# Kernel tuning notes

Measured on AMD Instinct MI355X. Metric: run time of the kernel, lower is better.

The kernel has to match this reference:

```python
import jax, jax.numpy as jnp
import numpy as np

CAPACITY_FACTOR = 1.0


def _top1_gate(x2d, wg):
    """GShard-style top-1 switch gate.
    x2d: [S, m], wg: [m, E] -> (l_aux, combine [S,E,C], dispatch [S,E,C])
    """
    S, _ = x2d.shape
    E = wg.shape[1]
    C = int(CAPACITY_FACTOR * S / E)  # expert capacity
    logits = x2d @ wg                              # [S, E]
    gates = jax.nn.softmax(logits, axis=-1)        # [S, E]
    idx = jnp.argmax(gates, axis=-1)               # [S]
    mask = jax.nn.one_hot(idx, E, dtype=jnp.int32) # [S, E]
    loc = jnp.cumsum(mask, axis=0) - 1             # position within each expert
    # load-balancing aux loss
    me = jnp.mean(gates, axis=0)
    ce = jnp.mean(mask.astype(gates.dtype), axis=0)
    l_aux = E * jnp.sum(me * ce)
    # drop tokens over capacity
    mask = mask * (loc < C).astype(jnp.int32)
    gate_s = jnp.sum(gates * mask, axis=-1)        # [S] gate value of kept token
    loc_s = jnp.sum(loc * mask, axis=-1)           # [S] slot index
    loc_oh = jax.nn.one_hot(loc_s, C, dtype=gates.dtype)          # [S, C]
    combine = (gate_s[:, None] * mask.astype(gates.dtype))[:, :, None] * loc_oh[:, None, :]  # [S,E,C]
    dispatch = (combine > 0).astype(gates.dtype)
    return l_aux, combine, dispatch


def setup_inputs() -> dict:
    key = jax.random.key(0)
    k1, k2, k3, k4 = jax.random.split(key, 4)
    s, b, m, E, ffn = 2048, 4, 1024, 8, 4096
    x = jax.random.normal(k1, (s, b, m), dtype=jnp.float32)
    wg = jax.random.normal(k2, (m, E), dtype=jnp.float32) * 0.02
    w1 = jax.random.normal(k3, (E, m, ffn), dtype=jnp.float32) * 0.02
    w2 = jax.random.normal(k4, (E, ffn, m), dtype=jnp.float32) * 0.02
    return {"x": x, "wg": wg, "w1": w1, "w2": w2}


def reference(x, wg, w1, w2):
    # world_size = 1, num_local_experts = E, num_prototypes z = 1
    s, b, m = x.shape
    x2d = x.reshape(-1, m)                          # [S, m]
    l_aux, combine, dispatch = _top1_gate(x2d, wg)  # [S,E,C]
    combine = combine[:, None]                      # [S, z=1, E, C]
    dispatch = dispatch[:, None]
    xr = x2d[:, None, :]                            # [S, z=1, m]
    # dense dispatch: szfc,szm->zfcm
    dispatched = jnp.einsum('szfc,szm->zfcm', dispatch, xr)
    # all-to-all with world_size=1 is identity; reshape to [E, C, m]
    E = w1.shape[0]
    di = dispatched.reshape(E, -1, m)               # [E, C, m]
    # experts: per-expert FFN with ReLU
    h = jax.nn.relu(jnp.einsum('ecm,emh->ech', di, w1))
    eo = jnp.einsum('ech,ehm->ecm', h, w2)          # [E, C, m]
    eo = eo[None]                                   # [z=1, E, C, m]
    out = jnp.einsum('szfc,zfcm->sm', combine, eo)  # [S, m]
    return out.reshape(s, b, m)
```

## Files before the change

kernel.cpp:

```cpp
#include <hip/hip_runtime.h>
#include <hip/hip_bf16.h>


#define NTOK 8192
#define DM   1024
#define NE   8
#define NF   4096
#define CAP  1024

typedef __bf16 bf16x8 __attribute__((ext_vector_type(8)));
typedef float  f32x4  __attribute__((ext_vector_type(4)));
typedef unsigned short us8v __attribute__((ext_vector_type(8)));

__device__ __forceinline__ unsigned short f2bf(float f) {
    union { float f; unsigned int u; } v; v.f = f;
    unsigned int u = v.u;
    return (unsigned short)((u + 0x7FFFu + ((u >> 16) & 1u)) >> 16);
}

__device__ __forceinline__ void async_cp16(const unsigned short* g, unsigned short* l) {
    __builtin_amdgcn_global_load_lds(
        (const __attribute__((address_space(1))) void*)g,
        (__attribute__((address_space(3))) void*)l, 16, 0, 0);
}

__global__ __launch_bounds__(256) void gate_kernel(
    const float* __restrict__ x, const float* __restrict__ wg,
    int* __restrict__ eid, float* __restrict__ gatev)
{
    int wave = threadIdx.x >> 6;
    int lane = threadIdx.x & 63;
    int t = blockIdx.x * 4 + wave;
    const float4* xr4 = (const float4*)(x + (size_t)t * DM);
    float acc[NE];
#pragma unroll
    for (int e = 0; e < NE; ++e) acc[e] = 0.f;
#pragma unroll
    for (int it = 0; it < 4; ++it) {
        int k4 = lane + it * 64;
        float4 xv = xr4[k4];
        float xc[4] = {xv.x, xv.y, xv.z, xv.w};
#pragma unroll
        for (int c = 0; c < 4; ++c) {
            const float4* wr = (const float4*)(wg + (size_t)(k4 * 4 + c) * NE);
            float4 w0 = wr[0], w1 = wr[1];
            acc[0] += xc[c] * w0.x; acc[1] += xc[c] * w0.y;
            acc[2] += xc[c] * w0.z; acc[3] += xc[c] * w0.w;
            acc[4] += xc[c] * w1.x; acc[5] += xc[c] * w1.y;
            acc[6] += xc[c] * w1.z; acc[7] += xc[c] * w1.w;
        }
    }
#pragma unroll
    for (int off = 32; off >= 1; off >>= 1) {
#pragma unroll
        for (int e = 0; e < NE; ++e) acc[e] += __shfl_xor(acc[e], off, 64);
    }
    if (lane == 0) {
        int best = 0; float bm = acc[0];
#pragma unroll
        for (int e = 1; e < NE; ++e) if (acc[e] > bm) { bm = acc[e]; best = e; }
        float ssum = 0.f;
#pragma unroll
        for (int e = 0; e < NE; ++e) ssum += __expf(acc[e] - bm);
        eid[t] = best;
        gatev[t] = 1.0f / ssum;
    }
}

__global__ __launch_bounds__(1024) void scan_kernel(
    const int* __restrict__ eid, int* __restrict__ slot_token)
{
    __shared__ int wtot[16][NE];
    int tid = threadIdx.x;
    int lane = tid & 63, wv = tid >> 6;
#pragma unroll
    for (int i = 0; i < 8; ++i) slot_token[tid + i * 1024] = -1;

    int el[8];
    int cnt[NE];
#pragma unroll
    for (int e = 0; e < NE; ++e) cnt[e] = 0;
#pragma unroll
    for (int i = 0; i < 8; ++i) {
        int e = eid[tid * 8 + i];
        el[i] = e;
        cnt[e]++;
    }
    int incl[NE];
#pragma unroll
    for (int e = 0; e < NE; ++e) incl[e] = cnt[e];
#pragma unroll
    for (int off = 1; off <= 32; off <<= 1) {
#pragma unroll
        for (int e = 0; e < NE; ++e) {
            int v = __shfl_up(incl[e], off, 64);
            if (lane >= off) incl[e] += v;
        }
    }
    if (lane == 63) {
#pragma unroll
        for (int e = 0; e < NE; ++e) wtot[wv][e] = incl[e];
    }
    __syncthreads();
    int base[NE];
#pragma unroll
    for (int e = 0; e < NE; ++e) {
        int s = 0;
        for (int w = 0; w < 16; ++w) s += (w < wv) ? wtot[w][e] : 0;
        base[e] = s + incl[e] - cnt[e];
    }
#pragma unroll
    for (int i = 0; i < 8; ++i) {
        int e = el[i];
        int loc = base[e]++;
        if (loc < CAP) slot_token[e * CAP + loc] = tid * 8 + i;
    }
}

template<int K, int N>
__global__ __launch_bounds__(256) void convT_kernel(
    const float* __restrict__ W, unsigned short* __restrict__ WT)
{
    __shared__ unsigned short tile[64][72];
    int e = blockIdx.z;
    int k0 = blockIdx.y * 64, n0 = blockIdx.x * 64;
    const float* Wp = W + (size_t)e * K * N;
    unsigned short* WTp = WT + (size_t)e * K * N;
    int tid = threadIdx.x;
    int cn = (tid & 15) * 4;
    int rk = tid >> 4;
#pragma unroll
    for (int i = 0; i < 4; ++i) {
        int k = rk + i * 16;
        float4 v = *(const float4*)(Wp + (size_t)(k0 + k) * N + n0 + cn);
        tile[cn + 0][k] = f2bf(v.x);
        tile[cn + 1][k] = f2bf(v.y);
        tile[cn + 2][k] = f2bf(v.z);
        tile[cn + 3][k] = f2bf(v.w);
    }
    __syncthreads();
    int ck = (tid & 7) * 8;
    int rn = tid >> 3;
#pragma unroll
    for (int i = 0; i < 2; ++i) {
        int n = rn + i * 32;
        us8v o = *(const us8v*)(&tile[n][ck]);
        *(us8v*)(WTp + (size_t)(n0 + n) * K + k0 + ck) = o;
    }
}

__global__ __launch_bounds__(256) void gather_kernel(
    const float* __restrict__ x, const int* __restrict__ slot_token,
    unsigned short* __restrict__ Xd)
{
    int tid = threadIdx.x;
    int local = tid & 127;
    int slot = blockIdx.x * 2 + (tid >> 7);
    int t = slot_token[slot];
    int c = local * 8;
    us8v o;
    if (t >= 0) {
        const float4* p = (const float4*)(x + (size_t)t * DM + c);
        float4 v0 = p[0], v1 = p[1];
        o[0] = f2bf(v0.x); o[1] = f2bf(v0.y); o[2] = f2bf(v0.z); o[3] = f2bf(v0.w);
        o[4] = f2bf(v1.x); o[5] = f2bf(v1.y); o[6] = f2bf(v1.z); o[7] = f2bf(v1.w);
    } else {
#pragma unroll
        for (int c8 = 0; c8 < 8; ++c8) o[c8] = 0;
    }
    *(us8v*)(Xd + (size_t)slot * DM + c) = o;
}

template<int K, int JF, int SLABS>
__device__ __forceinline__ void gemm_core(
    const unsigned short* __restrict__ Ab, const unsigned short* __restrict__ Bb,
    unsigned short* As, unsigned short* Bs, f32x4 acc[4][JF])
{
    int tid = threadIdx.x;
    int wave = tid >> 6, lane = tid & 63;
    int wr = (wave >> 1) * 64;
    int wc = (wave & 1) * (JF * 16);
#pragma unroll
    for (int i = 0; i < 4; ++i)
#pragma unroll
        for (int j = 0; j < JF; ++j) acc[i][j] = (f32x4){0.f, 0.f, 0.f, 0.f};

    int srow = lane >> 2;
    int gcq  = (((lane & 3) ^ ((lane >> 3) & 3))) * 8;
    int pcq  = (((lane >> 4) ^ ((lane >> 1) & 3))) * 8;
    int rfrag = lane & 15;

    for (int kt = 0; kt < K; kt += 32 * SLABS) {
#pragma unroll
        for (int h = 0; h < SLABS; ++h) {
#pragma unroll
            for (int i = 0; i < 2; ++i) {
                int q = wave * 2 + i;
                int row = q * 16 + srow;
                async_cp16(Ab + (size_t)row * K + kt + h * 32 + gcq,
                           As + h * 4096 + q * 512);
            }
#pragma unroll
            for (int i = 0; i < JF / 2; ++i) {
                int q = wave * (JF / 2) + i;
                int row = q * 16 + srow;
                async_cp16(Bb + (size_t)row * K + kt + h * 32 + gcq,
                           Bs + h * (JF * 1024) + q * 512);
            }
        }
        __syncthreads();
#pragma unroll
        for (int h = 0; h < SLABS; ++h) {
            bf16x8 af[4], bfr[JF];
#pragma unroll
            for (int i = 0; i < 4; ++i)
                af[i] = *(const bf16x8*)(As + h * 4096 + (wr + i * 16 + rfrag) * 32 + pcq);
#pragma unroll
            for (int j = 0; j < JF; ++j)
                bfr[j] = *(const bf16x8*)(Bs + h * (JF * 1024) + (wc + j * 16 + rfrag) * 32 + pcq);
#pragma unroll
            for (int i = 0; i < 4; ++i)
#pragma unroll
                for (int j = 0; j < JF; ++j)
                    acc[i][j] = __builtin_amdgcn_mfma_f32_16x16x32_bf16(af[i], bfr[j], acc[i][j], 0, 0, 0);
        }
        __syncthreads();
    }
}

__global__ __launch_bounds__(256, 2) void gemm1_kernel(
    const unsigned short* __restrict__ Xd, const unsigned short* __restrict__ W1T,
    unsigned short* __restrict__ H)
{
    __shared__ unsigned short smem[8192];
    unsigned short* As = smem;
    unsigned short* Bs = smem + 4096;
    int e = blockIdx.z;
    const unsigned short* Ab = Xd + ((size_t)e * CAP + blockIdx.y * 128) * DM;
    const unsigned short* Bb = W1T + ((size_t)e * NF + blockIdx.x * 128) * DM;
    f32x4 acc[4][4];
    gemm_core<DM, 4, 1>(Ab, Bb, As, Bs, acc);

    int tid = threadIdx.x, wave = tid >> 6, lane = tid & 63;
    int wc = (wave & 1) * 64;
    size_t Hrow0 = ((size_t)e * CAP + blockIdx.y * 128) * NF + blockIdx.x * 128;
    unsigned short* buf = smem;
#pragma unroll
    for (int p = 0; p < 2; ++p) {
        if ((wave >> 1) == p) {
#pragma unroll
            for (int i = 0; i < 4; ++i) {
#pragma unroll
                for (int j = 0; j < 4; ++j) {
                    int col = wc + j * 16 + (lane & 15);
#pragma unroll
                    for (int f = 0; f < 4; ++f) {
                        int lr = i * 16 + (lane >> 4) * 4 + f;
                        float v = acc[i][j][f];
                        v = v > 0.f ? v : 0.f;
                        buf[lr * 128 + col] = f2bf(v);
                    }
                }
            }
        }
        __syncthreads();
#pragma unroll
        for (int v = 0; v < 4; ++v) {
            int sidx = tid + v * 256;
            int r = sidx >> 4, seg = sidx & 15;
            us8v o = *(const us8v*)(buf + r * 128 + seg * 8);
            *(us8v*)(H + Hrow0 + (size_t)(p * 64 + r) * NF + seg * 8) = o;
        }
        __syncthreads();
    }
}

__global__ __launch_bounds__(256, 4) void gemm2_kernel(
    const unsigned short* __restrict__ H, const unsigned short* __restrict__ W2T,
    const int* __restrict__ slot_token, const float* __restrict__ gatev,
    float* __restrict__ out)
{
    __shared__ unsigned short As[2 * 4096];
    __shared__ unsigned short Bs[2 * 2048];
    int e = blockIdx.z;
    const unsigned short* Ab = H + ((size_t)e * CAP + blockIdx.y * 128) * NF;
    const unsigned short* Bb = W2T + ((size_t)e * DM + blockIdx.x * 64) * NF;
    f32x4 acc[4][2];
    gemm_core<NF, 2, 2>(Ab, Bb, As, Bs, acc);

    int tid = threadIdx.x, wave = tid >> 6, lane = tid & 63;
    int wr = (wave >> 1) * 64, wc = (wave & 1) * 32;
    int slot0 = e * CAP + blockIdx.y * 128;
#pragma unroll
    for (int i = 0; i < 4; ++i) {
        int rbase = wr + i * 16 + (lane >> 4) * 4;
#pragma unroll
        for (int f = 0; f < 4; ++f) {
            int row = rbase + f;
            int t = slot_token[slot0 + row];
            if (t >= 0) {
                float g = gatev[t];
#pragma unroll
                for (int j = 0; j < 2; ++j) {
                    int col = blockIdx.x * 64 + wc + j * 16 + (lane & 15);
                    out[(size_t)t * DM + col] = acc[i][j][f] * g;
                }
            }
        }
    }
}

extern "C" void kernel_launch(void* const* d_in, const int* in_sizes, int n_in,
                              void* d_out, int out_size, void* d_ws, size_t ws_size,
                              hipStream_t stream)
{
    const float* x  = (const float*)d_in[0];
    const float* wg = (const float*)d_in[1];
    const float* w1 = (const float*)d_in[2];
    const float* w2 = (const float*)d_in[3];
    float* out = (float*)d_out;

    char* ws = (char*)d_ws;
    size_t o = 0;
    auto nxt = [&](size_t b) { size_t r = o; o += (b + 255) & ~(size_t)255; return r; };
    int*   eid        = (int*)  (ws + nxt((size_t)NTOK * 4));
    float* gatev      = (float*)(ws + nxt((size_t)NTOK * 4));
    int*   slot_token = (int*)  (ws + nxt((size_t)NTOK * 4));
    unsigned short* Xd = (unsigned short*)(ws + nxt((size_t)NTOK * DM * 2));
    unsigned short* WT = (unsigned short*)(ws + nxt((size_t)NE * NF * DM * 2));
    unsigned short* Hb = (unsigned short*)(ws + nxt((size_t)NE * CAP * NF * 2));

    gate_kernel<<<NTOK / 4, 256, 0, stream>>>(x, wg, eid, gatev);
    scan_kernel<<<1, 1024, 0, stream>>>(eid, slot_token);
    convT_kernel<DM, NF><<<dim3(NF / 64, DM / 64, NE), 256, 0, stream>>>(w1, WT);
    gather_kernel<<<NTOK / 2, 256, 0, stream>>>(x, slot_token, Xd);
    gemm1_kernel<<<dim3(NF / 128, CAP / 128, NE), 256, 0, stream>>>(Xd, WT, Hb);
    convT_kernel<NF, DM><<<dim3(DM / 64, NF / 64, NE), 256, 0, stream>>>(w2, WT);
    hipMemsetAsync(d_out, 0, (size_t)out_size * sizeof(float), stream);
    gemm2_kernel<<<dim3(DM / 64, CAP / 128, NE), 256, 0, stream>>>(Hb, WT, slot_token, gatev, out);
}
```

Before: 564.7 us.

## Fuse gate, weight conversions and zeroing into one kernel; double-buffer GEMM loads

Gate computation, both weight transpose/bf16 conversions and output zeroing are merged into a single large launch when workspace allows, removing several launch gaps and the memset. The GEMM core gets a double-buffered LDS pipeline that issues the next k-slab's async copies before computing the current one, replacing the load-sync-compute loop. gemm1 occupancy hint changes from 2 to 3. The fused path needs a second weight buffer in workspace and doubles LDS use in gemm1.

```diff
diff --git a/kernel.cpp b/kernel.cpp
--- a/kernel.cpp
+++ b/kernel.cpp
@@ -24,13 +24,13 @@
         (__attribute__((address_space(3))) void*)l, 16, 0, 0);
 }
 
-__global__ __launch_bounds__(256) void gate_kernel(
-    const float* __restrict__ x, const float* __restrict__ wg,
+__device__ __forceinline__ void gate_body(
+    int bx, const float* __restrict__ x, const float* __restrict__ wg,
     int* __restrict__ eid, float* __restrict__ gatev)
 {
     int wave = threadIdx.x >> 6;
     int lane = threadIdx.x & 63;
-    int t = blockIdx.x * 4 + wave;
+    int t = bx * 4 + wave;
     const float4* xr4 = (const float4*)(x + (size_t)t * DM);
     float acc[NE];
 #pragma unroll
@@ -43,11 +43,11 @@
 #pragma unroll
         for (int c = 0; c < 4; ++c) {
             const float4* wr = (const float4*)(wg + (size_t)(k4 * 4 + c) * NE);
-            float4 w0 = wr[0], w1 = wr[1];
+            float4 w0 = wr[0], w1v = wr[1];
             acc[0] += xc[c] * w0.x; acc[1] += xc[c] * w0.y;
             acc[2] += xc[c] * w0.z; acc[3] += xc[c] * w0.w;
-            acc[4] += xc[c] * w1.x; acc[5] += xc[c] * w1.y;
-            acc[6] += xc[c] * w1.z; acc[7] += xc[c] * w1.w;
+            acc[4] += xc[c] * w1v.x; acc[5] += xc[c] * w1v.y;
+            acc[6] += xc[c] * w1v.z; acc[7] += xc[c] * w1v.w;
         }
     }
 #pragma unroll
@@ -67,63 +67,16 @@
     }
 }
 
-__global__ __launch_bounds__(1024) void scan_kernel(
-    const int* __restrict__ eid, int* __restrict__ slot_token)
-{
-    __shared__ int wtot[16][NE];
-    int tid = threadIdx.x;
-    int lane = tid & 63, wv = tid >> 6;
-#pragma unroll
-    for (int i = 0; i < 8; ++i) slot_token[tid + i * 1024] = -1;
-
-    int el[8];
-    int cnt[NE];
-#pragma unroll
-    for (int e = 0; e < NE; ++e) cnt[e] = 0;
-#pragma unroll
-    for (int i = 0; i < 8; ++i) {
-        int e = eid[tid * 8 + i];
-        el[i] = e;
-        cnt[e]++;
-    }
-    int incl[NE];
-#pragma unroll
-    for (int e = 0; e < NE; ++e) incl[e] = cnt[e];
-#pragma unroll
-    for (int off = 1; off <= 32; off <<= 1) {
-#pragma unroll
-        for (int e = 0; e < NE; ++e) {
-            int v = __shfl_up(incl[e], off, 64);
-            if (lane >= off) incl[e] += v;
-        }
-    }
-    if (lane == 63) {
-#pragma unroll
-        for (int e = 0; e < NE; ++e) wtot[wv][e] = incl[e];
-    }
-    __syncthreads();
-    int base[NE];
-#pragma unroll
-    for (int e = 0; e < NE; ++e) {
-        int s = 0;
-        for (int w = 0; w < 16; ++w) s += (w < wv) ? wtot[w][e] : 0;
-        base[e] = s + incl[e] - cnt[e];
-    }
-#pragma unroll
-    for (int i = 0; i < 8; ++i) {
-        int e = el[i];
-        int loc = base[e]++;
-        if (loc < CAP) slot_token[e * CAP + loc] = tid * 8 + i;
-    }
-}
-
 template<int K, int N>
-__global__ __launch_bounds__(256) void convT_kernel(
-    const float* __restrict__ W, unsigned short* __restrict__ WT)
-{
-    __shared__ unsigned short tile[64][72];
-    int e = blockIdx.z;
-    int k0 = blockIdx.y * 64, n0 = blockIdx.x * 64;
+__device__ __forceinline__ void convT_body(
+    const float* __restrict__ W, unsigned short* __restrict__ WT,
+    int idx, unsigned short (*tile)[72])
+{
+    constexpr int NX = N / 64;
+    int e = idx >> 10;
+    int rem = idx & 1023;
+    int n0 = (rem % NX) * 64;
+    int k0 = (rem / NX) * 64;
     const float* Wp = W + (size_t)e * K * N;
     unsigned short* WTp = WT + (size_t)e * K * N;
     int tid = threadIdx.x;
@@ -146,6 +99,88 @@
         int n = rn + i * 32;
         us8v o = *(const us8v*)(&tile[n][ck]);
         *(us8v*)(WTp + (size_t)(n0 + n) * K + k0 + ck) = o;
+    }
+}
+
+__global__ __launch_bounds__(256) void mega_kernel(
+    const float* __restrict__ x, const float* __restrict__ wg,
+    const float* __restrict__ w1, const float* __restrict__ w2,
+    int* __restrict__ eid, float* __restrict__ gatev,
+    unsigned short* __restrict__ W1T, unsigned short* __restrict__ W2T,
+    float* __restrict__ out)
+{
+    __shared__ unsigned short tile[64][72];
+    int bx = blockIdx.x;
+    if (bx < 2048) {
+        gate_body(bx, x, wg, eid, gatev);
+    } else if (bx < 10240) {
+        convT_body<DM, NF>(w1, W1T, bx - 2048, tile);
+    } else if (bx < 12288) {
+        size_t base = ((size_t)(bx - 10240) * 256 + threadIdx.x) * 16;
+        float4 z = {0.f, 0.f, 0.f, 0.f};
+        float4* p = (float4*)(out + base);
+        p[0] = z; p[1] = z; p[2] = z; p[3] = z;
+    } else {
+        convT_body<NF, DM>(w2, W2T, bx - 12288, tile);
+    }
+}
+
+template<int K, int N>
+__global__ __launch_bounds__(256) void convT_kernel(
+    const float* __restrict__ W, unsigned short* __restrict__ WT)
+{
+    __shared__ unsigned short tile[64][72];
+    int idx = (blockIdx.z << 10) | (blockIdx.y * (N / 64) + blockIdx.x);
+    convT_body<K, N>(W, WT, idx, tile);
+}
+
+__global__ __launch_bounds__(1024) void scan_kernel(
+    const int* __restrict__ eid, int* __restrict__ slot_token)
+{
+    __shared__ int wtot[16][NE];
+    int tid = threadIdx.x;
+    int lane = tid & 63, wv = tid >> 6;
+#pragma unroll
+    for (int i = 0; i < 8; ++i) slot_token[tid + i * 1024] = -1;
+
+    int el[8];
+    int cnt[NE];
+#pragma unroll
+    for (int e = 0; e < NE; ++e) cnt[e] = 0;
+#pragma unroll
+    for (int i = 0; i < 8; ++i) {
+        int e = eid[tid * 8 + i];
+        el[i] = e;
+        cnt[e]++;
+    }
+    int incl[NE];
+#pragma unroll
+    for (int e = 0; e < NE; ++e) incl[e] = cnt[e];
+#pragma unroll
+    for (int off = 1; off <= 32; off <<= 1) {
+#pragma unroll
+        for (int e = 0; e < NE; ++e) {
+            int v = __shfl_up(incl[e], off, 64);
+            if (lane >= off) incl[e] += v;
+        }
+    }
+    if (lane == 63) {
+#pragma unroll
+        for (int e = 0; e < NE; ++e) wtot[wv][e] = incl[e];
+    }
+    __syncthreads();
+    int base[NE];
+#pragma unroll
+    for (int e = 0; e < NE; ++e) {
+        int s = 0;
+        for (int w = 0; w < 16; ++w) s += (w < wv) ? wtot[w][e] : 0;
+        base[e] = s + incl[e] - cnt[e];
+    }
+#pragma unroll
+    for (int i = 0; i < 8; ++i) {
+        int e = el[i];
+        int loc = base[e]++;
+        if (loc < CAP) slot_token[e * CAP + loc] = tid * 8 + i;
     }
 }
 
@@ -171,8 +206,8 @@
     *(us8v*)(Xd + (size_t)slot * DM + c) = o;
 }
 
-template<int K, int JF, int SLABS>
-__device__ __forceinline__ void gemm_core(
+template<int K, int JF>
+__device__ __forceinline__ void gemm_core_db(
     const unsigned short* __restrict__ Ab, const unsigned short* __restrict__ Bb,
     unsigned short* As, unsigned short* Bs, f32x4 acc[4][JF])
 {
@@ -186,65 +221,65 @@
         for (int j = 0; j < JF; ++j) acc[i][j] = (f32x4){0.f, 0.f, 0.f, 0.f};
 
     int srow = lane >> 2;
-    int gcq  = (((lane & 3) ^ ((lane >> 3) & 3))) * 8;
-    int pcq  = (((lane >> 4) ^ ((lane >> 1) & 3))) * 8;
+    int gcq  = ((lane & 3) ^ ((lane >> 3) & 3)) * 8;
+    int pcq  = ((lane >> 4) ^ ((lane >> 1) & 3)) * 8;
     int rfrag = lane & 15;
-
-    for (int kt = 0; kt < K; kt += 32 * SLABS) {
-#pragma unroll
-        for (int h = 0; h < SLABS; ++h) {
-#pragma unroll
-            for (int i = 0; i < 2; ++i) {
-                int q = wave * 2 + i;
-                int row = q * 16 + srow;
-                async_cp16(Ab + (size_t)row * K + kt + h * 32 + gcq,
-                           As + h * 4096 + q * 512);
-            }
-#pragma unroll
-            for (int i = 0; i < JF / 2; ++i) {
-                int q = wave * (JF / 2) + i;
-                int row = q * 16 + srow;
-                async_cp16(Bb + (size_t)row * K + kt + h * 32 + gcq,
-                           Bs + h * (JF * 1024) + q * 512);
-            }
-        }
+    constexpr int S = K / 32;
+
+    auto issue = [&](int s) {
+        int slot = s & 1;
+        int kt = s * 32;
+#pragma unroll
+        for (int i = 0; i < 2; ++i) {
+            int q = wave * 2 + i;
+            int row = q * 16 + srow;
+            async_cp16(Ab + (size_t)row * K + kt + gcq, As + slot * 4096 + q * 512);
+        }
+#pragma unroll
+        for (int i = 0; i < JF / 2; ++i) {
+            int q = wave * (JF / 2) + i;
+            int row = q * 16 + srow;
+            async_cp16(Bb + (size_t)row * K + kt + gcq, Bs + slot * (JF * 1024) + q * 512);
+        }
+    };
+
+    issue(0);
+    for (int s = 0; s < S; ++s) {
         __syncthreads();
-#pragma unroll
-        for (int h = 0; h < SLABS; ++h) {
-            bf16x8 af[4], bfr[JF];
-#pragma unroll
-            for (int i = 0; i < 4; ++i)
-                af[i] = *(const bf16x8*)(As + h * 4096 + (wr + i * 16 + rfrag) * 32 + pcq);
+        if (s + 1 < S) issue(s + 1);
+        int slot = s & 1;
+        bf16x8 af[4], bfr[JF];
+#pragma unroll
+        for (int i = 0; i < 4; ++i)
+            af[i] = *(const bf16x8*)(As + slot * 4096 + (wr + i * 16 + rfrag) * 32 + pcq);
+#pragma unroll
+        for (int j = 0; j < JF; ++j)
+            bfr[j] = *(const bf16x8*)(Bs + slot * (JF * 1024) + (wc + j * 16 + rfrag) * 32 + pcq);
+#pragma unroll
+        for (int i = 0; i < 4; ++i)
 #pragma unroll
             for (int j = 0; j < JF; ++j)
-                bfr[j] = *(const bf16x8*)(Bs + h * (JF * 1024) + (wc + j * 16 + rfrag) * 32 + pcq);
-#pragma unroll
-            for (int i = 0; i < 4; ++i)
-#pragma unroll
-                for (int j = 0; j < JF; ++j)
-                    acc[i][j] = __builtin_amdgcn_mfma_f32_16x16x32_bf16(af[i], bfr[j], acc[i][j], 0, 0, 0);
-        }
-        __syncthreads();
-    }
-}
-
-__global__ __launch_bounds__(256, 2) void gemm1_kernel(
+                acc[i][j] = __builtin_amdgcn_mfma_f32_16x16x32_bf16(af[i], bfr[j], acc[i][j], 0, 0, 0);
+    }
+}
+
+__global__ __launch_bounds__(256, 3) void gemm1_kernel(
     const unsigned short* __restrict__ Xd, const unsigned short* __restrict__ W1T,
     unsigned short* __restrict__ H)
 {
-    __shared__ unsigned short smem[8192];
-    unsigned short* As = smem;
-    unsigned short* Bs = smem + 4096;
+    __shared__ unsigned short As[2 * 4096];
+    __shared__ unsigned short Bs[2 * 4096];
     int e = blockIdx.z;
     const unsigned short* Ab = Xd + ((size_t)e * CAP + blockIdx.y * 128) * DM;
     const unsigned short* Bb = W1T + ((size_t)e * NF + blockIdx.x * 128) * DM;
     f32x4 acc[4][4];
-    gemm_core<DM, 4, 1>(Ab, Bb, As, Bs, acc);
+    gemm_core_db<DM, 4>(Ab, Bb, As, Bs, acc);
 
     int tid = threadIdx.x, wave = tid >> 6, lane = tid & 63;
     int wc = (wave & 1) * 64;
     size_t Hrow0 = ((size_t)e * CAP + blockIdx.y * 128) * NF + blockIdx.x * 128;
-    unsigned short* buf = smem;
+    unsigned short* buf = As;
+    __syncthreads();
 #pragma unroll
     for (int p = 0; p < 2; ++p) {
         if ((wave >> 1) == p) {
@@ -286,7 +321,7 @@
     const unsigned short* Ab = H + ((size_t)e * CAP + blockIdx.y * 128) * NF;
     const unsigned short* Bb = W2T + ((size_t)e * DM + blockIdx.x * 64) * NF;
     f32x4 acc[4][2];
-    gemm_core<NF, 2, 2>(Ab, Bb, As, Bs, acc);
+    gemm_core_db<NF, 2>(Ab, Bb, As, Bs, acc);
 
     int tid = threadIdx.x, wave = tid >> 6, lane = tid & 63;
     int wr = (wave >> 1) * 64, wc = (wave & 1) * 32;
@@ -326,16 +361,27 @@
     int*   eid        = (int*)  (ws + nxt((size_t)NTOK * 4));
     float* gatev      = (float*)(ws + nxt((size_t)NTOK * 4));
     int*   slot_token = (int*)  (ws + nxt((size_t)NTOK * 4));
-    unsigned short* Xd = (unsigned short*)(ws + nxt((size_t)NTOK * DM * 2));
-    unsigned short* WT = (unsigned short*)(ws + nxt((size_t)NE * NF * DM * 2));
-    unsigned short* Hb = (unsigned short*)(ws + nxt((size_t)NE * CAP * NF * 2));
-
-    gate_kernel<<<NTOK / 4, 256, 0, stream>>>(x, wg, eid, gatev);
-    scan_kernel<<<1, 1024, 0, stream>>>(eid, slot_token);
-    convT_kernel<DM, NF><<<dim3(NF / 64, DM / 64, NE), 256, 0, stream>>>(w1, WT);
-    gather_kernel<<<NTOK / 2, 256, 0, stream>>>(x, slot_token, Xd);
-    gemm1_kernel<<<dim3(NF / 128, CAP / 128, NE), 256, 0, stream>>>(Xd, WT, Hb);
-    convT_kernel<NF, DM><<<dim3(DM / 64, NF / 64, NE), 256, 0, stream>>>(w2, WT);
-    hipMemsetAsync(d_out, 0, (size_t)out_size * sizeof(float), stream);
-    gemm2_kernel<<<dim3(DM / 64, CAP / 128, NE), 256, 0, stream>>>(Hb, WT, slot_token, gatev, out);
-}
+    unsigned short* Xd  = (unsigned short*)(ws + nxt((size_t)NTOK * DM * 2));
+    unsigned short* W1T = (unsigned short*)(ws + nxt((size_t)NE * NF * DM * 2));
+    unsigned short* Hb  = (unsigned short*)(ws + nxt((size_t)NE * CAP * NF * 2));
+    size_t need_fused = o + (size_t)NE * NF * DM * 2;
+    bool fused = ws_size >= need_fused;
+    unsigned short* W2T = fused
+        ? (unsigned short*)(ws + nxt((size_t)NE * NF * DM * 2))
+        : W1T;
+
+    if (fused) {
+        mega_kernel<<<20480, 256, 0, stream>>>(x, wg, w1, w2, eid, gatev, W1T, W2T, out);
+        scan_kernel<<<1, 1024, 0, stream>>>(eid, slot_token);
+        gather_kernel<<<NTOK / 2, 256, 0, stream>>>(x, slot_token, Xd);
+        gemm1_kernel<<<dim3(NF / 128, CAP / 128, NE), 256, 0, stream>>>(Xd, W1T, Hb);
+        gemm2_kernel<<<dim3(DM / 64, CAP / 128, NE), 256, 0, stream>>>(Hb, W2T, slot_token, gatev, out);
+    } else {
+        mega_kernel<<<12288, 256, 0, stream>>>(x, wg, w1, w2, eid, gatev, W1T, W2T, out);
+        scan_kernel<<<1, 1024, 0, stream>>>(eid, slot_token);
+        gather_kernel<<<NTOK / 2, 256, 0, stream>>>(x, slot_token, Xd);
+        gemm1_kernel<<<dim3(NF / 128, CAP / 128, NE), 256, 0, stream>>>(Xd, W1T, Hb);
+        convT_kernel<NF, DM><<<dim3(DM / 64, NF / 64, NE), 256, 0, stream>>>(w2, W2T);
+        gemm2_kernel<<<dim3(DM / 64, CAP / 128, NE), 256, 0, stream>>>(Hb, W2T, slot_token, gatev, out);
+    }
+}
```

Measured after the change: 582.3 us. 3.1% more time.
